# Kernel tuning notes

Hardware: AMD Instinct MI355X
Metric: run time of the kernel (lower is better)

## Reference

```python
import jax, jax.numpy as jnp
import numpy as np

DIM = 1024
NUM_HEADS = 16
BATCH = 4
SEQ = 2048
SCALE = (DIM // NUM_HEADS) ** -0.5
MASK_VAL = -10000000.0


def setup_inputs() -> dict:
    key = jax.random.key(0)
    k1, k2, k3, k4 = jax.random.split(key, 4)
    inputs = jax.random.normal(k1, (BATCH, SEQ, DIM), dtype=jnp.float32)
    # xavier-ish scaling for weights
    W_qkv = jax.random.normal(k2, (3 * DIM, DIM), dtype=jnp.float32) * (1.0 / np.sqrt(DIM))
    W_fc = jax.random.normal(k3, (DIM, DIM), dtype=jnp.float32) * (1.0 / np.sqrt(DIM))
    b_fc = jnp.zeros((DIM,), dtype=jnp.float32)
    padding_mask = jax.random.randint(k4, (BATCH, SEQ), 0, 2, dtype=jnp.int32)
    return {"inputs": inputs, "W_qkv": W_qkv, "W_fc": W_fc, "b_fc": b_fc,
            "padding_mask": padding_mask}


def reference(inputs, W_qkv, W_fc, b_fc, padding_mask):
    B, N, C = inputs.shape
    H = NUM_HEADS
    Dh = C // H
    # qkv projection (torch Linear: x @ W.T), [B,N,3C]
    qkv = jnp.einsum('bnc,oc->bno', inputs, W_qkv)
    qkv = qkv.reshape(B, N, 3, H, Dh).transpose(2, 0, 3, 1, 4)  # [3,B,H,N,Dh]
    q, k, v = qkv[0], qkv[1], qkv[2]
    att = jnp.einsum('bhqd,bhkd->bhqk', q, k) * SCALE  # [B,H,N,N]
    mask = padding_mask[:, None, None, :]              # [B,1,1,N]
    att = jnp.where(mask > 0, jnp.float32(MASK_VAL), att)
    att = jax.nn.softmax(att, axis=-1)
    x = jnp.einsum('bhqk,bhkd->bhqd', att, v)          # [B,H,N,Dh]
    x = x.transpose(0, 2, 1, 3).reshape(B, N, C)       # [B,N,C]
    out = jnp.einsum('bnc,oc->bno', x, W_fc) + b_fc
    return out
```

## Files before the change

### kernel.cpp

```cpp
#include <hip/hip_runtime.h>
#include <stdint.h>

constexpr int kDim  = 1024;
constexpr int kH    = 16;
constexpr int kB    = 4;
constexpr int kSeq  = 2048;
constexpr int kDh   = 64;
constexpr int kMTot = kB * kSeq;
constexpr int kNQkv = 3 * kDim;
constexpr float kScale = 0.125f;
constexpr float kLog2e = 1.44269504088896f;
constexpr float kC1    = kScale * kLog2e;
constexpr float kMaxSub = 10.0f;
constexpr float kMk2Un   = -kMaxSub * kLog2e;
constexpr float kMk2Mask = -1.0e9f;
constexpr int kPld = 72;
constexpr int kCld = 136;

typedef __attribute__((ext_vector_type(8))) short short8;
typedef __attribute__((ext_vector_type(4))) float floatx4;

__device__ __forceinline__ unsigned short f2bf(float f) {
  union { float f; unsigned u; } v; v.f = f;
  unsigned r = v.u + 0x7fffu + ((v.u >> 16) & 1u);
  return (unsigned short)(r >> 16);
}
__device__ __forceinline__ unsigned short f2bf_fast(float f) {
  union { float f; unsigned u; } v; v.f = f;
  return (unsigned short)((v.u + 0x8000u) >> 16);
}
__device__ __forceinline__ float vexp2(float x) {
  float r; asm("v_exp_f32 %0, %1" : "=v"(r) : "v"(x)); return r;
}
__device__ __forceinline__ void gl2lds16(const void* g, void* l) {
  __builtin_amdgcn_global_load_lds(
      (const __attribute__((address_space(1))) unsigned int*)g,
      (__attribute__((address_space(3))) unsigned int*)l, 16, 0, 0);
}

__global__ void __launch_bounds__(256) cvt_scan(
    const float4* __restrict__ x, const float4* __restrict__ wq,
    const float4* __restrict__ wf,
    ushort4* __restrict__ xb, ushort4* __restrict__ wqb, ushort4* __restrict__ wfb,
    const int* __restrict__ pm, int* __restrict__ cidx, int* __restrict__ nkd,
    int* __restrict__ ctr) {
  const int X4  = (kMTot * kDim) / 4;
  const int WQ4 = (kNQkv * kDim) / 4;
  const int NCVT = 12288;
  if (blockIdx.x >= NCVT) {
    const int b = blockIdx.x - NCVT;
    const int t = threadIdx.x;
    const int lane = t & 63, wv = t >> 6;
    __shared__ int wsum[4];
    __shared__ int woff[5];
    if (b == 0 && t == 0) *ctr = 256;
    int base = t * 8;
    int keep[8]; int cnt = 0;
#pragma unroll
    for (int j = 0; j < 8; j++) {
      keep[j] = (pm[b * kSeq + base + j] <= 0) ? 1 : 0;
      cnt += keep[j];
    }
    int pre = cnt;
#pragma unroll
    for (int off = 1; off < 64; off <<= 1) {
      int v = __shfl_up(pre, off, 64);
      if (lane >= off) pre += v;
    }
    int excl = pre - cnt;
    if (lane == 63) wsum[wv] = pre;
    __syncthreads();
    if (t == 0) {
      int s = 0;
#pragma unroll
      for (int w = 0; w < 4; w++) { woff[w] = s; s += wsum[w]; }
      woff[4] = s;
      nkd[b] = s;
    }
    __syncthreads();
    const int nk = woff[4];
    int kp = woff[wv] + excl;
#pragma unroll
    for (int j = 0; j < 8; j++) {
      int n = base + j;
      int pos = keep[j] ? kp : nk + (n - kp);
      cidx[b * kSeq + pos] = b * kSeq + n;
      kp += keep[j];
    }
    return;
  }
  int i = blockIdx.x * 256 + threadIdx.x;
  float4 v; ushort4* dst;
  if (i < X4)            { v = x[i];             dst = xb  + i; }
  else if (i < X4 + WQ4) { v = wq[i - X4];       dst = wqb + (i - X4); }
  else                   { v = wf[i - X4 - WQ4]; dst = wfb + (i - X4 - WQ4); }
  ushort4 o;
  o.x = f2bf(v.x); o.y = f2bf(v.y); o.z = f2bf(v.z); o.w = f2bf(v.w);
  *dst = o;
}

__global__ void __launch_bounds__(512, 2) gemm_qkv(
    const unsigned short* __restrict__ xb, const unsigned short* __restrict__ wqb,
    const int* __restrict__ cidx, const int* __restrict__ nkd,
    int* __restrict__ ctr,
    unsigned short* __restrict__ qb, unsigned short* __restrict__ kb,
    unsigned short* __restrict__ vtb) {
  extern __shared__ __attribute__((aligned(16))) unsigned short smem[];
  __shared__ int s_slot;
  unsigned short* As0 = smem;
  unsigned short* Bs0 = smem + 16384;
  unsigned short* As1 = smem + 32768;
  unsigned short* Bs1 = smem + 49152;

  const int t = threadIdx.x;
  const int lane = t & 63, wv = t >> 6;
  const int wm = (wv >> 2) << 7;
  const int wn = (wv & 3) << 6;
  const int lrow = lane & 15, quad = lane >> 4, l7 = lane & 7;
  const int srow = t >> 3;
  const int pu8 = (t & 7) * 8;
  const int lu8 = ((t & 7) ^ (srow & 7)) * 8;
  const int off0 = (quad ^ l7) * 8;

  const int rr0 = (nkd[0] + 127) >> 7, rr1 = (nkd[1] + 127) >> 7;
  const int rr2 = (nkd[2] + 127) >> 7, rr3 = (nkd[3] + 127) >> 7;
  const int tb0 = (rr0 + 1) >> 1, tb1 = (rr1 + 1) >> 1;
  const int tb2 = (rr2 + 1) >> 1, tb3 = (rr3 + 1) >> 1;
  const int pA = tb0, pB = pA + tb1, pC = pB + tb2, pD = pC + tb3;
  const int NT = 128 + 8 * pD;

#define STAGE_B(buf, p, k0) gl2lds16(brow + (int64_t)(p) * 64 * kDim + (k0), \
                                     (buf) + ((p) * 64 + srow) * 64 + pu8)
#define STAGE_A(buf, p, k0) gl2lds16(arow[p] + (k0), \
                                     (buf) + ((p) * 64 + srow) * 64 + pu8)
#define BARRIER() { asm volatile("" ::: "memory"); \
                    __builtin_amdgcn_s_barrier(); \
                    asm volatile("" ::: "memory"); }

  int slot = blockIdx.x;
  while (slot < NT) {
    int which, tN, tMl, bb, rbv;
    if (slot < 128) {
      which = 0; tN = (slot & 3) * 256;
      int tMg = (slot >> 2) * 256;
      bb = tMg >> 11; tMl = tMg & 2047; rbv = 16;
    } else {
      int id = slot - 128;
      const int TK = 4 * pD;
      which = (id < TK) ? 1 : 2;
      if (which == 2) id -= TK;
      int col = id & 3, j = id >> 2;
      int pj;
      if (j < pA)      { bb = 0; pj = j;      rbv = rr0; }
      else if (j < pB) { bb = 1; pj = j - pA; rbv = rr1; }
      else if (j < pC) { bb = 2; pj = j - pB; rbv = rr2; }
      else             { bb = 3; pj = j - pC; rbv = rr3; }
      tMl = pj * 256;
      tN = (which == 1 ? 1024 : 2048) + col * 256;
    }
    int nrows;
    if (which == 0) nrows = 256;
    else { int rem = rbv * 128 - tMl; nrows = (rem >= 256) ? 256 : 128; }
    const bool na4 = (nrows == 256);
    const bool act = (wm < nrows);
    const bool vblk = (which == 2);

    const unsigned short* arow[4];
#pragma unroll
    for (int p = 0; p < 4; p++) {
      int pe = (!na4 && p > 1) ? 1 : p;
      int rl = tMl + pe * 64 + srow;
      int rid = (which == 0) ? (bb * 2048 + rl) : cidx[bb * 2048 + rl];
      arow[p] = xb + (int64_t)rid * kDim + lu8;
    }
    const unsigned short* brow = wqb + (int64_t)(tN + srow) * kDim + lu8;

    floatx4 acc[8][4];
    floatx4 zero = {0.f, 0.f, 0.f, 0.f};
#pragma unroll
    for (int mi = 0; mi < 8; mi++)
#pragma unroll
      for (int ni = 0; ni < 4; ni++) acc[mi][ni] = zero;

    STAGE_B(Bs0, 0, 0); STAGE_B(Bs0, 1, 0); STAGE_B(Bs0, 2, 0); STAGE_B(Bs0, 3, 0);
    STAGE_A(As0, 0, 0); STAGE_A(As0, 1, 0);
    if (na4) { STAGE_A(As0, 2, 0); STAGE_A(As0, 3, 0); }
    STAGE_B(Bs1, 0, 64); STAGE_B(Bs1, 1, 64); STAGE_B(Bs1, 2, 64); STAGE_B(Bs1, 3, 64);
    STAGE_A(As1, 0, 64); STAGE_A(As1, 1, 64);
    if (na4) { STAGE_A(As1, 2, 64); STAGE_A(As1, 3, 64); }
    if (na4) { asm volatile("s_waitcnt vmcnt(8)" ::: "memory"); }
    else     { asm volatile("s_waitcnt vmcnt(6)" ::: "memory"); }
    BARRIER();

    for (int tt = 0; tt < 16; ++tt) {
      const unsigned short* Ac = (tt & 1) ? As1 : As0;
      const unsigned short* Bc = (tt & 1) ? Bs1 : Bs0;
      unsigned short* An = (tt & 1) ? As0 : As1;
      unsigned short* Bn = (tt & 1) ? Bs0 : Bs1;

      if (tt >= 1 && tt < 15) {
        const int kn = (tt + 1) * 64;
        STAGE_B(Bn, 0, kn); STAGE_B(Bn, 1, kn); STAGE_B(Bn, 2, kn); STAGE_B(Bn, 3, kn);
        STAGE_A(An, 0, kn); STAGE_A(An, 1, kn);
        if (na4) { STAGE_A(An, 2, kn); STAGE_A(An, 3, kn); }
      }

      if (act) {
#pragma unroll
        for (int kk = 0; kk < 64; kk += 32) {
          short8 bf[4], af[8];
#pragma unroll
          for (int ni = 0; ni < 4; ni++)
            bf[ni] = *(const short8*)(Bc + (wn + ni * 16 + lrow) * 64 + (off0 ^ kk));
#pragma unroll
          for (int mi = 0; mi < 8; mi++)
            af[mi] = *(const short8*)(Ac + (wm + mi * 16 + lrow) * 64 + (off0 ^ kk));
#pragma unroll
          for (int mi = 0; mi < 8; mi++)
#pragma unroll
            for (int ni = 0; ni < 4; ni++)
              acc[mi][ni] = __builtin_amdgcn_mfma_f32_16x16x32_bf16(af[mi], bf[ni], acc[mi][ni], 0, 0, 0);
        }
      }

      asm volatile("s_waitcnt vmcnt(0)" ::: "memory");
      BARRIER();
    }

    unsigned short* Cs = smem;
    const int h4 = (tN >> 6) & 15;
#pragma unroll
    for (int h = 0; h < 2; h++) {
      const bool writer = ((((wv & 3) >> 1) == h) && act);
      const int cwn = (wv & 1) * 64;
      if (!vblk) {
        if (writer) {
#pragma unroll
          for (int mi = 0; mi < 8; mi++)
#pragma unroll
            for (int ni = 0; ni < 4; ni++)
#pragma unroll
              for (int r = 0; r < 4; r++) {
                int row = wm + mi * 16 + quad * 4 + r;
                int c = cwn + ni * 16 + lrow;
                Cs[row * kCld + c] = f2bf(acc[mi][ni][r]);
              }
        }
        asm volatile("s_waitcnt lgkmcnt(0)" ::: "memory");
        BARRIER();
        unsigned short* qk = (which == 0) ? qb : kb;
        const int itn = nrows >> 6;
#pragma unroll
        for (int g = 0; g < 2; g++) {
          int hh = (h4 + h * 2 + g) & 15;
          unsigned short* base = qk + ((int64_t)((bb << 4) + hh) << 17)
                                 + (int64_t)tMl * 64;
          for (int it = 0; it < itn; it++) {
            int off = it * 4096 + t * 8;
            int n = off >> 6;
            int d = off & 63;
            *(short8*)(base + off) = *(const short8*)(Cs + n * kCld + g * 64 + d);
          }
        }
        BARRIER();
      } else {
        if (writer) {
#pragma unroll
          for (int mi = 0; mi < 8; mi++)
#pragma unroll
            for (int ni = 0; ni < 4; ni++)
#pragma unroll
              for (int r = 0; r < 4; r++) {
                int row = wm + mi * 16 + quad * 4 + r;
                int c = cwn + ni * 16 + lrow;
                Cs[c * 264 + row] = f2bf(acc[mi][ni][r]);
              }
        }
        asm volatile("s_waitcnt lgkmcnt(0)" ::: "memory");
        BARRIER();
        const int c8n = nrows >> 3;
#pragma unroll
        for (int g = 0; g < 2; g++) {
          int hh = (h4 + h * 2 + g) & 15;
          unsigned short* vbase = vtb + (((int64_t)((bb << 4) + hh)) << 17) + tMl;
#pragma unroll
          for (int it = 0; it < 4; it++) {
            int off = it * 512 + t;
            int d = off >> 5, c8 = off & 31;
            if (c8 < c8n)
              *(short8*)(vbase + (int64_t)d * 2048 + c8 * 8) =
                  *(const short8*)(Cs + (g * 64 + d) * 264 + c8 * 8);
          }
        }
        BARRIER();
      }
    }

    if (t == 0) s_slot = atomicAdd(ctr, 1);
    __syncthreads();
    slot = s_slot;
  }
#undef STAGE_B
#undef STAGE_A
#undef BARRIER
}

__global__ void __launch_bounds__(256, 4) attn(
    const unsigned short* __restrict__ qb, const unsigned short* __restrict__ kb,
    const unsigned short* __restrict__ vtb, const int* __restrict__ nkd,
    unsigned short* __restrict__ xab) {
  __shared__ __attribute__((aligned(16))) unsigned short Ks[64 * 64];
  __shared__ __attribute__((aligned(16))) unsigned short Vs[64 * 64];
  __shared__ __attribute__((aligned(16))) unsigned short Ps[4][2][16 * kPld];

  const int t = threadIdx.x, lane = t & 63, wv = t >> 6;
  const int lrow = lane & 15, quad = lane >> 4, l7 = lane & 7;
  const int qblk = blockIdx.x & 15, bh = blockIdx.x >> 4;
  const int b = bh >> 4, h = bh & 15;
  const int q0 = qblk * 128;
  const int srow = t >> 3;
  const int pu8 = (t & 7) * 8;
  const int lu8 = ((t & 7) ^ (srow & 7)) * 8;
  const int off0 = (quad ^ l7) * 8;

  const int nk  = nkd[b];
  const int nkt = (nk + 63) >> 6;

  const unsigned short* Qb0 = qb + ((int64_t)bh * kSeq + q0 + wv * 16 + lrow) * kDh;
  short8 qf[2][2];
  qf[0][0] = *(const short8*)(Qb0 + quad * 8);
  qf[0][1] = *(const short8*)(Qb0 + 32 + quad * 8);
  qf[1][0] = *(const short8*)(Qb0 + 64 * kDh + quad * 8);
  qf[1][1] = *(const short8*)(Qb0 + 64 * kDh + 32 + quad * 8);

  float l_run[2][4];
  floatx4 o_acc[2][4];
  floatx4 zero = {0.f, 0.f, 0.f, 0.f};
#pragma unroll
  for (int t2 = 0; t2 < 2; t2++) {
#pragma unroll
    for (int r = 0; r < 4; r++) l_run[t2][r] = 0.f;
#pragma unroll
    for (int di = 0; di < 4; di++) o_acc[t2][di] = zero;
  }

  const unsigned short* Kbase = kb  + (int64_t)bh * kSeq * kDh;
  const unsigned short* Vbase = vtb + (int64_t)bh * kDh * kSeq;
  const int r0 = srow, r1 = srow + 32;

  gl2lds16(Kbase + (int64_t)r0 * kDh + lu8, Ks + r0 * 64 + pu8);
  gl2lds16(Kbase + (int64_t)r1 * kDh + lu8, Ks + r1 * 64 + pu8);
  gl2lds16(Vbase + (int64_t)r0 * kSeq + lu8, Vs + r0 * 64 + pu8);
  gl2lds16(Vbase + (int64_t)r1 * kSeq + lu8, Vs + r1 * 64 + pu8);
  asm volatile("s_waitcnt vmcnt(0)" ::: "memory");
  __syncthreads();

  for (int kt = 0; kt < nkt; ++kt) {
    const int k0 = kt * 64;
    const bool pf = (kt + 1 < nkt);
    short8 nkv0, nkv1, nvv0, nvv1;
    if (pf) {
      const int k1 = k0 + 64;
      nkv0 = *(const short8*)(Kbase + (int64_t)(k1 + r0) * kDh + lu8);
      nkv1 = *(const short8*)(Kbase + (int64_t)(k1 + r1) * kDh + lu8);
      nvv0 = *(const short8*)(Vbase + (int64_t)r0 * kSeq + k1 + lu8);
      nvv1 = *(const short8*)(Vbase + (int64_t)r1 * kSeq + k1 + lu8);
    }

    floatx4 s[2][4];
#pragma unroll
    for (int ni = 0; ni < 4; ni++) {
      const unsigned short* Kr = Ks + (ni * 16 + lrow) * 64;
      short8 kf0 = *(const short8*)(Kr + off0);
      short8 kf1 = *(const short8*)(Kr + (off0 ^ 32));
#pragma unroll
      for (int t2 = 0; t2 < 2; t2++) {
        floatx4 tmp = __builtin_amdgcn_mfma_f32_16x16x32_bf16(qf[t2][0], kf0, zero, 0, 0, 0);
        s[t2][ni]   = __builtin_amdgcn_mfma_f32_16x16x32_bf16(qf[t2][1], kf1, tmp, 0, 0, 0);
      }
    }
    float mk2[4];
#pragma unroll
    for (int c = 0; c < 4; c++)
      mk2[c] = (k0 + c * 16 + lrow < nk) ? kMk2Un : kMk2Mask;

#pragma unroll
    for (int t2 = 0; t2 < 2; t2++) {
      unsigned short* Pw = &Ps[wv][t2][0];
#pragma unroll
      for (int r = 0; r < 4; r++) {
        int prow = (quad * 4 + r) * kPld + lrow;
#pragma unroll
        for (int c = 0; c < 4; c++) {
          float p = vexp2(fmaf(s[t2][c][r], kC1, mk2[c]));
          l_run[t2][r] += p;
          Pw[prow + c * 16] = f2bf_fast(p);
        }
      }
    }
    asm volatile("s_waitcnt lgkmcnt(0)" ::: "memory");

#pragma unroll
    for (int ks = 0; ks < 2; ks++) {
      short8 pf0 = *(const short8*)(&Ps[wv][0][0] + lrow * kPld + ks * 32 + quad * 8);
      short8 pf1 = *(const short8*)(&Ps[wv][1][0] + lrow * kPld + ks * 32 + quad * 8);
      const int voff = off0 ^ (ks * 32);
#pragma unroll
      for (int di = 0; di < 4; di++) {
        short8 vf = *(const short8*)(Vs + (di * 16 + lrow) * 64 + voff);
        o_acc[0][di] = __builtin_amdgcn_mfma_f32_16x16x32_bf16(pf0, vf, o_acc[0][di], 0, 0, 0);
        o_acc[1][di] = __builtin_amdgcn_mfma_f32_16x16x32_bf16(pf1, vf, o_acc[1][di], 0, 0, 0);
      }
    }
    __syncthreads();

    if (pf) {
      *(short8*)(Ks + r0 * 64 + pu8) = nkv0;
      *(short8*)(Ks + r1 * 64 + pu8) = nkv1;
      *(short8*)(Vs + r0 * 64 + pu8) = nvv0;
      *(short8*)(Vs + r1 * 64 + pu8) = nvv1;
      __syncthreads();
    }
  }

#pragma unroll
  for (int t2 = 0; t2 < 2; t2++) {
#pragma unroll
    for (int r = 0; r < 4; r++) {
      float l = l_run[t2][r];
      l += __shfl_xor(l, 1, 64);
      l += __shfl_xor(l, 2, 64);
      l += __shfl_xor(l, 4, 64);
      l += __shfl_xor(l, 8, 64);
      float inv = 1.0f / l;
      int n = q0 + t2 * 64 + wv * 16 + quad * 4 + r;
      int64_t rowbase = ((int64_t)b * kSeq + n) * kDim + h * kDh;
#pragma unroll
      for (int di = 0; di < 4; di++)
        xab[rowbase + di * 16 + lrow] = f2bf(o_acc[t2][di][r] * inv);
    }
  }
}

__global__ void __launch_bounds__(256) gemm_fc(
    const unsigned short* __restrict__ xab, const unsigned short* __restrict__ wfb,
    const float* __restrict__ bfc, float* __restrict__ out) {
  __shared__ __attribute__((aligned(16))) unsigned short As[128 * 64];
  __shared__ __attribute__((aligned(16))) unsigned short Bs[128 * 64];
  const int tN = blockIdx.x * 128, tM = blockIdx.y * 128;
  const int t = threadIdx.x;
  const int lane = t & 63, wv = t >> 6;
  const int wm = (wv >> 1) << 6, wn = (wv & 1) << 6;
  const int lrow = lane & 15, quad = lane >> 4, l7 = lane & 7;
  const int srow = t >> 3;
  const int pu8 = (t & 7) * 8;
  const int lu8 = ((t & 7) ^ (srow & 7)) * 8;
  const int off0 = (quad ^ l7) * 8;

  floatx4 acc[4][4];
  floatx4 zero = {0.f, 0.f, 0.f, 0.f};
#pragma unroll
  for (int mi = 0; mi < 4; mi++)
#pragma unroll
    for (int ni = 0; ni < 4; ni++) acc[mi][ni] = zero;

  for (int k0 = 0; k0 < kDim; k0 += 64) {
#pragma unroll
    for (int p = 0; p < 4; ++p) {
      int r = srow + p * 32;
      gl2lds16(xab + (int64_t)(tM + r) * kDim + k0 + lu8, As + r * 64 + pu8);
      gl2lds16(wfb + (int64_t)(tN + r) * kDim + k0 + lu8, Bs + r * 64 + pu8);
    }
    __syncthreads();
#pragma unroll
    for (int kk = 0; kk < 64; kk += 32) {
      short8 af[4], bf[4];
#pragma unroll
      for (int mi = 0; mi < 4; mi++)
        af[mi] = *(const short8*)(As + (wm + mi * 16 + lrow) * 64 + (off0 ^ kk));
#pragma unroll
      for (int ni = 0; ni < 4; ni++)
        bf[ni] = *(const short8*)(Bs + (wn + ni * 16 + lrow) * 64 + (off0 ^ kk));
#pragma unroll
      for (int mi = 0; mi < 4; mi++)
#pragma unroll
        for (int ni = 0; ni < 4; ni++)
          acc[mi][ni] = __builtin_amdgcn_mfma_f32_16x16x32_bf16(af[mi], bf[ni], acc[mi][ni], 0, 0, 0);
    }
    __syncthreads();
  }

#pragma unroll
  for (int ni = 0; ni < 4; ni++) {
    int o = tN + wn + ni * 16 + lrow;
    float bias = bfc[o];
#pragma unroll
    for (int mi = 0; mi < 4; mi++) {
#pragma unroll
      for (int r = 0; r < 4; r++) {
        int i = tM + wm + mi * 16 + quad * 4 + r;
        out[(int64_t)i * kDim + o] = acc[mi][ni][r] + bias;
      }
    }
  }
}

extern "C" void kernel_launch(void* const* d_in, const int* in_sizes, int n_in,
                              void* d_out, int out_size, void* d_ws, size_t ws_size,
                              hipStream_t stream) {
  (void)in_sizes; (void)n_in; (void)out_size; (void)ws_size;
  const float* x    = (const float*)d_in[0];
  const float* wqkv = (const float*)d_in[1];
  const float* wfc  = (const float*)d_in[2];
  const float* bfc  = (const float*)d_in[3];
  const int*   pm   = (const int*)d_in[4];
  float* out = (float*)d_out;

  char* ws = (char*)d_ws;
  unsigned short* xb  = (unsigned short*)(ws);
  unsigned short* wqb = (unsigned short*)(ws + 16777216);
  unsigned short* wfb = (unsigned short*)(ws + 23068672);
  unsigned short* qb  = (unsigned short*)(ws + 25165824);
  unsigned short* kb  = (unsigned short*)(ws + 41943040);
  unsigned short* vtb = (unsigned short*)(ws + 58720256);
  int*            cidx= (int*)(ws + 75497472);
  int*            nkd = (int*)(ws + 75530240);
  int*            ctr = (int*)(ws + 75530256);
  unsigned short* xab = xb;

  static bool s_attr_set = false;
  if (!s_attr_set) {
    (void)hipFuncSetAttribute((const void*)gemm_qkv,
                              hipFuncAttributeMaxDynamicSharedMemorySize, 131072);
    s_attr_set = true;
  }

  cvt_scan<<<12288 + kB, 256, 0, stream>>>(
      (const float4*)x, (const float4*)wqkv, (const float4*)wfc,
      (ushort4*)xb, (ushort4*)wqb, (ushort4*)wfb, pm, cidx, nkd, ctr);
  gemm_qkv<<<256, 512, 131072, stream>>>(
      xb, wqb, cidx, nkd, ctr, qb, kb, vtb);
  attn<<<kB * kH * (kSeq / 128), 256, 0, stream>>>(qb, kb, vtb, nkd, xab);
  gemm_fc<<<dim3(kDim / 128, kMTot / 128), 256, 0, stream>>>(xab, wfb, bfc, out);
}
```

Measured before the change: 240.9 us.

## Double-buffer FC GEMM with 256x128 tiles and 512-thread blocks

Rewrites the output projection GEMM to use 256x128 tiles computed by 8 waves, with two LDS buffers so the next K-slice loads while the current one is multiplied. Raw s_barrier with explicit vmcnt waits replaces the full __syncthreads. The grid becomes 256 blocks, one per CU, to remove the wave-quantization tail and overlap global loads with MFMA. The cost is larger LDS use and fewer resident blocks. Accumulator register pressure stays the same.

```diff
diff --git a/kernel.cpp b/kernel.cpp
--- a/kernel.cpp
+++ b/kernel.cpp
@@ -442,60 +442,91 @@
   }
 }
 
-__global__ void __launch_bounds__(256) gemm_fc(
+__global__ void __launch_bounds__(512, 2) gemm_fc(
     const unsigned short* __restrict__ xab, const unsigned short* __restrict__ wfb,
     const float* __restrict__ bfc, float* __restrict__ out) {
-  __shared__ __attribute__((aligned(16))) unsigned short As[128 * 64];
-  __shared__ __attribute__((aligned(16))) unsigned short Bs[128 * 64];
-  const int tN = blockIdx.x * 128, tM = blockIdx.y * 128;
+  extern __shared__ __attribute__((aligned(16))) unsigned short smem[];
+  unsigned short* As0 = smem;
+  unsigned short* Bs0 = smem + 16384;
+  unsigned short* As1 = smem + 24576;
+  unsigned short* Bs1 = smem + 40960;
+
   const int t = threadIdx.x;
   const int lane = t & 63, wv = t >> 6;
-  const int wm = (wv >> 1) << 6, wn = (wv & 1) << 6;
+  const int wm = (wv >> 2) << 7;
+  const int wn = (wv & 3) << 5;
   const int lrow = lane & 15, quad = lane >> 4, l7 = lane & 7;
   const int srow = t >> 3;
   const int pu8 = (t & 7) * 8;
   const int lu8 = ((t & 7) ^ (srow & 7)) * 8;
   const int off0 = (quad ^ l7) * 8;
 
-  floatx4 acc[4][4];
+  const int task = blockIdx.x;
+  const int tM = (task >> 3) * 256;
+  const int tN = (task & 7) * 128;
+
+  const unsigned short* arow = xab + (int64_t)(tM + srow) * kDim + lu8;
+  const unsigned short* brow = wfb + (int64_t)(tN + srow) * kDim + lu8;
+
+#define BARRIER() { asm volatile("" ::: "memory"); \
+                    __builtin_amdgcn_s_barrier(); \
+                    asm volatile("" ::: "memory"); }
+#define STAGE_T(Abuf, Bbuf, k0) { \
+    gl2lds16(arow + 0 * 64 * kDim + (k0), (Abuf) + (0 * 64 + srow) * 64 + pu8); \
+    gl2lds16(arow + 1 * 64 * kDim + (k0), (Abuf) + (1 * 64 + srow) * 64 + pu8); \
+    gl2lds16(arow + 2 * 64 * kDim + (k0), (Abuf) + (2 * 64 + srow) * 64 + pu8); \
+    gl2lds16(arow + 3 * 64 * kDim + (k0), (Abuf) + (3 * 64 + srow) * 64 + pu8); \
+    gl2lds16(brow + 0 * 64 * kDim + (k0), (Bbuf) + (0 * 64 + srow) * 64 + pu8); \
+    gl2lds16(brow + 1 * 64 * kDim + (k0), (Bbuf) + (1 * 64 + srow) * 64 + pu8); }
+
+  floatx4 acc[8][2];
   floatx4 zero = {0.f, 0.f, 0.f, 0.f};
 #pragma unroll
-  for (int mi = 0; mi < 4; mi++)
-#pragma unroll
-    for (int ni = 0; ni < 4; ni++) acc[mi][ni] = zero;
-
-  for (int k0 = 0; k0 < kDim; k0 += 64) {
-#pragma unroll
-    for (int p = 0; p < 4; ++p) {
-      int r = srow + p * 32;
-      gl2lds16(xab + (int64_t)(tM + r) * kDim + k0 + lu8, As + r * 64 + pu8);
-      gl2lds16(wfb + (int64_t)(tN + r) * kDim + k0 + lu8, Bs + r * 64 + pu8);
-    }
-    __syncthreads();
+  for (int mi = 0; mi < 8; mi++)
+#pragma unroll
+    for (int ni = 0; ni < 2; ni++) acc[mi][ni] = zero;
+
+  STAGE_T(As0, Bs0, 0);
+  STAGE_T(As1, Bs1, 64);
+  asm volatile("s_waitcnt vmcnt(6)" ::: "memory");
+  BARRIER();
+
+  for (int tt = 0; tt < 16; ++tt) {
+    const unsigned short* Ac = (tt & 1) ? As1 : As0;
+    const unsigned short* Bc = (tt & 1) ? Bs1 : Bs0;
+    unsigned short* An = (tt & 1) ? As0 : As1;
+    unsigned short* Bn = (tt & 1) ? Bs0 : Bs1;
+
+    if (tt >= 1 && tt < 15) STAGE_T(An, Bn, (tt + 1) * 64);
+
 #pragma unroll
     for (int kk = 0; kk < 64; kk += 32) {
-      short8 af[4], bf[4];
-#pragma unroll
-      for (int mi = 0; mi < 4; mi++)
-        af[mi] = *(const short8*)(As + (wm + mi * 16 + lrow) * 64 + (off0 ^ kk));
-#pragma unroll
-      for (int ni = 0; ni < 4; ni++)
-        bf[ni] = *(const short8*)(Bs + (wn + ni * 16 + lrow) * 64 + (off0 ^ kk));
-#pragma unroll
-      for (int mi = 0; mi < 4; mi++)
-#pragma unroll
-        for (int ni = 0; ni < 4; ni++)
+      short8 bf[2], af[8];
+#pragma unroll
+      for (int ni = 0; ni < 2; ni++)
+        bf[ni] = *(const short8*)(Bc + (wn + ni * 16 + lrow) * 64 + (off0 ^ kk));
+#pragma unroll
+      for (int mi = 0; mi < 8; mi++)
+        af[mi] = *(const short8*)(Ac + (wm + mi * 16 + lrow) * 64 + (off0 ^ kk));
+#pragma unroll
+      for (int mi = 0; mi < 8; mi++)
+#pragma unroll
+        for (int ni = 0; ni < 2; ni++)
           acc[mi][ni] = __builtin_amdgcn_mfma_f32_16x16x32_bf16(af[mi], bf[ni], acc[mi][ni], 0, 0, 0);
     }
-    __syncthreads();
-  }
-
-#pragma unroll
-  for (int ni = 0; ni < 4; ni++) {
+
+    asm volatile("s_waitcnt vmcnt(0)" ::: "memory");
+    BARRIER();
+  }
+#undef STAGE_T
+#undef BARRIER
+
+#pragma unroll
+  for (int ni = 0; ni < 2; ni++) {
     int o = tN + wn + ni * 16 + lrow;
     float bias = bfc[o];
 #pragma unroll
-    for (int mi = 0; mi < 4; mi++) {
+    for (int mi = 0; mi < 8; mi++) {
 #pragma unroll
       for (int r = 0; r < 4; r++) {
         int i = tM + wm + mi * 16 + quad * 4 + r;
@@ -532,6 +563,8 @@
   if (!s_attr_set) {
     (void)hipFuncSetAttribute((const void*)gemm_qkv,
                               hipFuncAttributeMaxDynamicSharedMemorySize, 131072);
+    (void)hipFuncSetAttribute((const void*)gemm_fc,
+                              hipFuncAttributeMaxDynamicSharedMemorySize, 98304);
     s_attr_set = true;
   }
 
@@ -541,5 +574,5 @@
   gemm_qkv<<<256, 512, 131072, stream>>>(
       xb, wqb, cidx, nkd, ctr, qb, kb, vtb);
   attn<<<kB * kH * (kSeq / 128), 256, 0, stream>>>(qb, kb, vtb, nkd, xab);
-  gemm_fc<<<dim3(kDim / 128, kMTot / 128), 256, 0, stream>>>(xab, wfb, bfc, out);
-}
+  gemm_fc<<<256, 512, 98304, stream>>>(xab, wfb, bfc, out);
+}
```

Result: no change. 244.6 us (+1.5%).
